# Kernel tuning notes

Hardware: AMD Instinct MI355X
Metric: run time of the kernel (lower is better)

The kernel has to match this reference:

```python
import jax, jax.numpy as jnp
import numpy as np

K = 7        # local attention window (kernel_size)
PAD = 3      # (K-1)//2, keeps spatial dims
GROUPS = 8   # attention heads


def _unfold(t, k, H, W):
    """t: [B,C,H+k-1,W+k-1] -> [B,C,H,W,k,k] sliding-window patches (stride 1).
    Matches torch .unfold(2,k,1).unfold(3,k,1): first k over height offsets,
    second k over width offsets."""
    cols = [t[:, :, i:i + H, j:j + W] for i in range(k) for j in range(k)]
    p = jnp.stack(cols, axis=-1)  # [B,C,H,W,k*k]
    return p.reshape(t.shape[0], t.shape[1], H, W, k, k)


def setup_inputs() -> dict:
    key = jax.random.key(0)
    ks = jax.random.split(key, 6)
    B, C, O, H, Wd = 4, 128, 128, 64, 64
    x = jax.random.normal(ks[0], (B, C, H, Wd), dtype=jnp.float32)
    # 1x1 conv weights, kaiming normal fan_out (fan_out = O for 1x1)
    scale = (2.0 / O) ** 0.5
    Wq = jax.random.normal(ks[1], (O, C), dtype=jnp.float32) * scale
    Wk = jax.random.normal(ks[2], (O, C), dtype=jnp.float32) * scale
    Wv = jax.random.normal(ks[3], (O, C), dtype=jnp.float32) * scale
    rel_h = jax.random.normal(ks[4], (O // 2, 1, 1, K, 1), dtype=jnp.float32)
    rel_w = jax.random.normal(ks[5], (O // 2, 1, 1, 1, K), dtype=jnp.float32)
    return {"x": x, "Wq": Wq, "Wk": Wk, "Wv": Wv, "rel_h": rel_h, "rel_w": rel_w}


def reference(x, Wq, Wk, Wv, rel_h, rel_w):
    B, C, H, W = x.shape
    O = Wq.shape[0]
    g = GROUPS
    # 1x1 convs (no bias)
    q = jnp.einsum('bchw,oc->bohw', x, Wq)                    # [B,O,H,W]
    xp = jnp.pad(x, ((0, 0), (0, 0), (PAD, PAD), (PAD, PAD)))
    k = jnp.einsum('bchw,oc->bohw', xp, Wk)                   # [B,O,Hp,Wp]
    v = jnp.einsum('bchw,oc->bohw', xp, Wv)
    kp = _unfold(k, K, H, W)                                  # [B,O,H,W,K,K]
    vp = _unfold(v, K, H, W)
    # relative position embeddings: height on first half of channels, width on second
    kh, kw = jnp.split(kp, 2, axis=1)
    kp = jnp.concatenate([kh + rel_h, kw + rel_w], axis=1)    # [B,O,H,W,K,K]
    kp = kp.reshape(B, g, O // g, H, W, K * K)
    vp = vp.reshape(B, g, O // g, H, W, K * K)
    qg = q.reshape(B, g, O // g, H, W, 1)
    scores = (qg * kp).sum(axis=2)                            # [B,g,H,W,K*K]
    attn = jax.nn.softmax(scores, axis=-1)
    out = jnp.einsum('bghwn,bgchwn->bgchw', attn, vp)         # [B,g,O/g,H,W]
    return out.reshape(B, O, H, W)
```

## Files before the change

kernel.cpp:

```cpp
#include <hip/hip_runtime.h>
#include <hip/hip_bf16.h>

#define B_   4
#define C_   128
#define H_   64
#define W_   64
#define HW_  4096
#define KW_  7
#define PAD_ 3
#define G_   8
#define CPG_ 16

#define CPAD 136

#define TS    16
#define HALO  22
#define NHP   (HALO*HALO)
#define LP    24

typedef _Float16 f16x8 __attribute__((ext_vector_type(8)));
typedef _Float16 h2    __attribute__((ext_vector_type(2)));
typedef float    f32x4 __attribute__((ext_vector_type(4)));

static __device__ __forceinline__ unsigned short f2h(float f) {
    _Float16 h = (_Float16)f;
    union { _Float16 h; unsigned short u; } cv; cv.h = h;
    return cv.u;
}

#if defined(__has_builtin)
#if __has_builtin(__builtin_amdgcn_fdot2)
#define HAVE_FDOT2 1
#endif
#endif

__global__ __launch_bounds__(256) void proj_mfma(
    const float* __restrict__ x,
    const float* __restrict__ Wq,
    const float* __restrict__ Wk,
    const float* __restrict__ Wv,
    unsigned short* __restrict__ qkv16)
{
    const int ptile = blockIdx.x;
    const int b     = blockIdx.y;
    const int m     = blockIdx.z;
    const float* Wm = (m == 0) ? Wq : ((m == 1) ? Wk : Wv);
    const float* xb = x + (size_t)b * C_ * HW_;
    unsigned short* y = qkv16 + ((size_t)(m * B_ + b)) * HW_ * C_;
    const int p0  = ptile * 64;
    const int tid = threadIdx.x;

    __shared__ unsigned short wls[128 * CPAD];
    __shared__ unsigned short xls[64 * CPAD];

    #pragma unroll
    for (int it = 0; it < 16; ++it) {
        const int idx = tid + it * 256;
        const int o   = idx >> 5;
        const int c4  = (idx & 31) * 4;
        const float4 w4 = *(const float4*)(Wm + (size_t)o * C_ + c4);
        ushort4 hh;
        hh.x = f2h(w4.x); hh.y = f2h(w4.y); hh.z = f2h(w4.z); hh.w = f2h(w4.w);
        *(ushort4*)(&wls[o * CPAD + c4]) = hh;
    }
    #pragma unroll
    for (int it = 0; it < 2; ++it) {
        const int idx = tid + it * 256;
        const int pq  = (idx & 15) * 4;
        const int cq  = (idx >> 4) * 4;
        const float* xp = xb + (size_t)cq * HW_ + p0 + pq;
        const float4 r0 = *(const float4*)(xp);
        const float4 r1 = *(const float4*)(xp + HW_);
        const float4 r2 = *(const float4*)(xp + 2 * HW_);
        const float4 r3 = *(const float4*)(xp + 3 * HW_);
        ushort4 hh;
        hh.x = f2h(r0.x); hh.y = f2h(r1.x); hh.z = f2h(r2.x); hh.w = f2h(r3.x);
        *(ushort4*)(&xls[(pq + 0) * CPAD + cq]) = hh;
        hh.x = f2h(r0.y); hh.y = f2h(r1.y); hh.z = f2h(r2.y); hh.w = f2h(r3.y);
        *(ushort4*)(&xls[(pq + 1) * CPAD + cq]) = hh;
        hh.x = f2h(r0.z); hh.y = f2h(r1.z); hh.z = f2h(r2.z); hh.w = f2h(r3.z);
        *(ushort4*)(&xls[(pq + 2) * CPAD + cq]) = hh;
        hh.x = f2h(r0.w); hh.y = f2h(r1.w); hh.z = f2h(r2.w); hh.w = f2h(r3.w);
        *(ushort4*)(&xls[(pq + 3) * CPAD + cq]) = hh;
    }
    __syncthreads();

    const int wv   = tid >> 6;
    const int lane = tid & 63;
    const int row  = lane & 15;
    const int kq   = lane >> 4;

    f32x4 acc[8];
    #pragma unroll
    for (int ot = 0; ot < 8; ++ot)
        acc[ot] = (f32x4){0.f, 0.f, 0.f, 0.f};

    #pragma unroll
    for (int ks = 0; ks < 4; ++ks) {
        const int cb = ks * 32 + kq * 8;
        const f16x8 bfrag = *(const f16x8*)(&xls[(wv * 16 + row) * CPAD + cb]);
        #pragma unroll
        for (int ot = 0; ot < 8; ++ot) {
            const f16x8 afrag = *(const f16x8*)(&wls[(ot * 16 + row) * CPAD + cb]);
            acc[ot] = __builtin_amdgcn_mfma_f32_16x16x32_f16(afrag, bfrag, acc[ot], 0, 0, 0);
        }
    }

    const int p = p0 + wv * 16 + row;
    #pragma unroll
    for (int ot = 0; ot < 8; ++ot) {
        ushort4 hh;
        hh.x = f2h(acc[ot][0]); hh.y = f2h(acc[ot][1]);
        hh.z = f2h(acc[ot][2]); hh.w = f2h(acc[ot][3]);
        *(ushort4*)(y + ((size_t)ot * HW_ + p) * CPG_ + kq * 4) = hh;
    }
}

__global__ __launch_bounds__(256) void attn_kernel(
    const unsigned short* __restrict__ qkv16,
    const float* __restrict__ rel_h,
    const float* __restrict__ rel_w,
    float* __restrict__ out)
{
    const int tile = blockIdx.x;
    const int g    = blockIdx.y;
    const int b    = blockIdx.z;
    const int h0   = (tile >> 2) * TS;
    const int w0   = (tile & 3) * TS;
    const int c0   = g * CPG_;

    __shared__ unsigned short kvls[2][NHP * LP];

    const size_t gplane = (size_t)HW_ * CPG_;
    const size_t mplane = (size_t)B_ * G_ * gplane;
    const unsigned short* qb = qkv16              + ((size_t)b * G_ + g) * gplane;
    const unsigned short* kb = qkv16 + mplane     + ((size_t)b * G_ + g) * gplane;
    const unsigned short* vb = qkv16 + 2 * mplane + ((size_t)b * G_ + g) * gplane;

    const int tid = threadIdx.x;
    const int pw  = tid & 15;
    const int ph  = tid >> 4;
    const int pix = (h0 + ph) * W_ + (w0 + pw);

    const f16x8 q0 = *(const f16x8*)(qb + (size_t)pix * CPG_);
    const f16x8 q1 = *(const f16x8*)(qb + (size_t)pix * CPG_ + 8);

    #pragma unroll
    for (int it = 0; it < 8; ++it) {
        const int idx = tid + it * 256;
        if (idx < 2 * NHP * 2) {
            const int arr  = (idx >= NHP * 2) ? 1 : 0;
            const int r    = idx - arr * NHP * 2;
            const int lp   = r >> 1;
            const int half = r & 1;
            const int hy   = h0 + lp / HALO - PAD_;
            const int hx   = w0 + lp % HALO - PAD_;
            f16x8 val = (f16x8)(_Float16)0.f;
            if ((unsigned)hy < (unsigned)H_ && (unsigned)hx < (unsigned)W_) {
                const unsigned short* src = (arr ? vb : kb)
                    + (size_t)(hy * W_ + hx) * CPG_ + half * 8;
                val = *(const f16x8*)src;
            }
            *(f16x8*)(&kvls[arr][lp * LP + half * 8]) = val;
        }
    }

    float qv[CPG_];
    #pragma unroll
    for (int c = 0; c < 8; ++c) { qv[c] = (float)q0[c]; qv[8 + c] = (float)q1[c]; }

    const bool useH = (g < 4);
    const float* rp = useH ? (rel_h + c0 * KW_) : (rel_w + (c0 - 64) * KW_);
    float rel[KW_];
    #pragma unroll
    for (int t = 0; t < KW_; ++t) {
        float r = 0.f;
        #pragma unroll
        for (int c = 0; c < CPG_; ++c) r += qv[c] * rp[c * KW_ + t];
        rel[t] = r;
    }

    __syncthreads();

    float s[KW_ * KW_];
    float smax = -1e30f;
    #pragma unroll
    for (int i = 0; i < KW_; ++i) {
        #pragma unroll
        for (int j = 0; j < KW_; ++j) {
            const unsigned short* kp = &kvls[0][((ph + i) * HALO + (pw + j)) * LP];
            const f16x8 k0 = *(const f16x8*)(kp);
            const f16x8 k1 = *(const f16x8*)(kp + 8);
            float sc = useH ? rel[i] : rel[j];
#ifdef HAVE_FDOT2
            #pragma unroll
            for (int t = 0; t < 4; ++t) {
                sc = __builtin_amdgcn_fdot2((h2){q0[2*t], q0[2*t+1]},
                                            (h2){k0[2*t], k0[2*t+1]}, sc, false);
                sc = __builtin_amdgcn_fdot2((h2){q1[2*t], q1[2*t+1]},
                                            (h2){k1[2*t], k1[2*t+1]}, sc, false);
            }
#else
            #pragma unroll
            for (int c = 0; c < 8; ++c)
                sc += qv[c] * (float)k0[c] + qv[8 + c] * (float)k1[c];
#endif
            s[i * KW_ + j] = sc;
            smax = fmaxf(smax, sc);
        }
    }

    float denom = 0.f;
    #pragma unroll
    for (int n = 0; n < KW_ * KW_; ++n) {
        s[n] = __expf(s[n] - smax);
        denom += s[n];
    }
    const float rdenom = 1.f / denom;

    float acc[CPG_];
    #pragma unroll
    for (int c = 0; c < CPG_; ++c) acc[c] = 0.f;
    #pragma unroll
    for (int i = 0; i < KW_; ++i) {
        #pragma unroll
        for (int j = 0; j < KW_; ++j) {
            const float a = s[i * KW_ + j];
            const unsigned short* vp = &kvls[1][((ph + i) * HALO + (pw + j)) * LP];
            const f16x8 v0 = *(const f16x8*)(vp);
            const f16x8 v1 = *(const f16x8*)(vp + 8);
            #pragma unroll
            for (int c = 0; c < 8; ++c) {
                acc[c]     += a * (float)v0[c];
                acc[8 + c] += a * (float)v1[c];
            }
        }
    }

    float* ob = out + ((size_t)b * C_ + c0) * HW_;
    #pragma unroll
    for (int c = 0; c < CPG_; ++c)
        ob[(size_t)c * HW_ + pix] = acc[c] * rdenom;
}

extern "C" void kernel_launch(void* const* d_in, const int* in_sizes, int n_in,
                              void* d_out, int out_size, void* d_ws, size_t ws_size,
                              hipStream_t stream) {
    const float* x     = (const float*)d_in[0];
    const float* Wq    = (const float*)d_in[1];
    const float* Wk    = (const float*)d_in[2];
    const float* Wv    = (const float*)d_in[3];
    const float* rel_h = (const float*)d_in[4];
    const float* rel_w = (const float*)d_in[5];
    unsigned short* ws = (unsigned short*)d_ws;
    float* out = (float*)d_out;

    dim3 gA(HW_ / 64, B_, 3);
    proj_mfma<<<gA, 256, 0, stream>>>(x, Wq, Wk, Wv, ws);

    dim3 gB(16, G_, B_);
    attn_kernel<<<gB, 256, 0, stream>>>(ws, rel_h, rel_w, out);
}
```

Baseline: 33.16 us.

## Compute two vertically adjacent pixels per thread to reuse K/V LDS loads

The attention kernel now uses 128 threads per block, with each thread handling two vertically adjacent output pixels. The K and V rows it loads from shared memory are reused across both pixels' overlapping 7x7 windows, cutting LDS reads per output roughly in half. In exchange, register use per thread roughly doubles (two score arrays and two accumulators) and there are fewer waves per block, which may lower occupancy or cause spills.

```diff
diff --git a/kernel.cpp b/kernel.cpp
--- a/kernel.cpp
+++ b/kernel.cpp
@@ -116,7 +116,7 @@
     }
 }
 
-__global__ __launch_bounds__(256) void attn_kernel(
+__global__ __launch_bounds__(128) void attn_kernel(
     const unsigned short* __restrict__ qkv16,
     const float* __restrict__ rel_h,
     const float* __restrict__ rel_w,
@@ -129,7 +129,8 @@
     const int w0   = (tile & 3) * TS;
     const int c0   = g * CPG_;
 
-    __shared__ unsigned short kvls[2][NHP * LP];
+    __shared__ unsigned short kls[NHP * LP];
+    __shared__ unsigned short vls[NHP * LP];
 
     const size_t gplane = (size_t)HW_ * CPG_;
     const size_t mplane = (size_t)B_ * G_ * gplane;
@@ -139,15 +140,19 @@
 
     const int tid = threadIdx.x;
     const int pw  = tid & 15;
-    const int ph  = tid >> 4;
-    const int pix = (h0 + ph) * W_ + (w0 + pw);
-
-    const f16x8 q0 = *(const f16x8*)(qb + (size_t)pix * CPG_);
-    const f16x8 q1 = *(const f16x8*)(qb + (size_t)pix * CPG_ + 8);
-
-    #pragma unroll
-    for (int it = 0; it < 8; ++it) {
-        const int idx = tid + it * 256;
+    const int php = tid >> 4;
+    const int row0 = 2 * php;
+    const int pix0 = (h0 + row0) * W_ + (w0 + pw);
+    const int pix1 = pix0 + W_;
+
+    const f16x8 q0a = *(const f16x8*)(qb + (size_t)pix0 * CPG_);
+    const f16x8 q0b = *(const f16x8*)(qb + (size_t)pix0 * CPG_ + 8);
+    const f16x8 q1a = *(const f16x8*)(qb + (size_t)pix1 * CPG_);
+    const f16x8 q1b = *(const f16x8*)(qb + (size_t)pix1 * CPG_ + 8);
+
+    #pragma unroll
+    for (int it = 0; it < 16; ++it) {
+        const int idx = tid + it * 128;
         if (idx < 2 * NHP * 2) {
             const int arr  = (idx >= NHP * 2) ? 1 : 0;
             const int r    = idx - arr * NHP * 2;
@@ -161,86 +166,184 @@
                     + (size_t)(hy * W_ + hx) * CPG_ + half * 8;
                 val = *(const f16x8*)src;
             }
-            *(f16x8*)(&kvls[arr][lp * LP + half * 8]) = val;
-        }
-    }
-
-    float qv[CPG_];
-    #pragma unroll
-    for (int c = 0; c < 8; ++c) { qv[c] = (float)q0[c]; qv[8 + c] = (float)q1[c]; }
+            unsigned short* dst = (arr ? vls : kls) + lp * LP + half * 8;
+            *(f16x8*)dst = val;
+        }
+    }
 
     const bool useH = (g < 4);
     const float* rp = useH ? (rel_h + c0 * KW_) : (rel_w + (c0 - 64) * KW_);
-    float rel[KW_];
-    #pragma unroll
-    for (int t = 0; t < KW_; ++t) {
-        float r = 0.f;
-        #pragma unroll
-        for (int c = 0; c < CPG_; ++c) r += qv[c] * rp[c * KW_ + t];
-        rel[t] = r;
+    float rel0[KW_], rel1[KW_];
+    {
+        float qv0[CPG_], qv1[CPG_];
+        #pragma unroll
+        for (int c = 0; c < 8; ++c) {
+            qv0[c] = (float)q0a[c]; qv0[8 + c] = (float)q0b[c];
+            qv1[c] = (float)q1a[c]; qv1[8 + c] = (float)q1b[c];
+        }
+        #pragma unroll
+        for (int t = 0; t < KW_; ++t) {
+            float r0 = 0.f, r1 = 0.f;
+            #pragma unroll
+            for (int c = 0; c < CPG_; ++c) {
+                const float w = rp[c * KW_ + t];
+                r0 += qv0[c] * w;
+                r1 += qv1[c] * w;
+            }
+            rel0[t] = r0; rel1[t] = r1;
+        }
     }
 
     __syncthreads();
 
-    float s[KW_ * KW_];
-    float smax = -1e30f;
-    #pragma unroll
-    for (int i = 0; i < KW_; ++i) {
+    float s0[KW_ * KW_], s1[KW_ * KW_];
+    #pragma unroll
+    for (int i = 0; i < KW_; ++i)
         #pragma unroll
         for (int j = 0; j < KW_; ++j) {
-            const unsigned short* kp = &kvls[0][((ph + i) * HALO + (pw + j)) * LP];
-            const f16x8 k0 = *(const f16x8*)(kp);
-            const f16x8 k1 = *(const f16x8*)(kp + 8);
-            float sc = useH ? rel[i] : rel[j];
+            s0[i * KW_ + j] = useH ? rel0[i] : rel0[j];
+            s1[i * KW_ + j] = useH ? rel1[i] : rel1[j];
+        }
+
+    #pragma unroll
+    for (int r = 0; r < 8; ++r) {
+        const int base = ((row0 + r) * HALO + pw) * LP;
+        {
+            f16x8 ka[KW_];
+            #pragma unroll
+            for (int t = 0; t < KW_; ++t)
+                ka[t] = *(const f16x8*)(&kls[base + t * LP]);
+            if (r < 7) {
+                #pragma unroll
+                for (int j = 0; j < KW_; ++j) {
+                    float sc = s0[r * KW_ + j];
 #ifdef HAVE_FDOT2
-            #pragma unroll
-            for (int t = 0; t < 4; ++t) {
-                sc = __builtin_amdgcn_fdot2((h2){q0[2*t], q0[2*t+1]},
-                                            (h2){k0[2*t], k0[2*t+1]}, sc, false);
-                sc = __builtin_amdgcn_fdot2((h2){q1[2*t], q1[2*t+1]},
-                                            (h2){k1[2*t], k1[2*t+1]}, sc, false);
-            }
+                    #pragma unroll
+                    for (int t = 0; t < 4; ++t)
+                        sc = __builtin_amdgcn_fdot2((h2){q0a[2*t], q0a[2*t+1]},
+                                                    (h2){ka[j][2*t], ka[j][2*t+1]}, sc, false);
 #else
-            #pragma unroll
-            for (int c = 0; c < 8; ++c)
-                sc += qv[c] * (float)k0[c] + qv[8 + c] * (float)k1[c];
-#endif
-            s[i * KW_ + j] = sc;
-            smax = fmaxf(smax, sc);
-        }
-    }
-
-    float denom = 0.f;
+                    #pragma unroll
+                    for (int c = 0; c < 8; ++c) sc += (float)q0a[c] * (float)ka[j][c];
+#endif
+                    s0[r * KW_ + j] = sc;
+                }
+            }
+            if (r >= 1) {
+                #pragma unroll
+                for (int j = 0; j < KW_; ++j) {
+                    float sc = s1[(r - 1) * KW_ + j];
+#ifdef HAVE_FDOT2
+                    #pragma unroll
+                    for (int t = 0; t < 4; ++t)
+                        sc = __builtin_amdgcn_fdot2((h2){q1a[2*t], q1a[2*t+1]},
+                                                    (h2){ka[j][2*t], ka[j][2*t+1]}, sc, false);
+#else
+                    #pragma unroll
+                    for (int c = 0; c < 8; ++c) sc += (float)q1a[c] * (float)ka[j][c];
+#endif
+                    s1[(r - 1) * KW_ + j] = sc;
+                }
+            }
+        }
+        {
+            f16x8 kb2[KW_];
+            #pragma unroll
+            for (int t = 0; t < KW_; ++t)
+                kb2[t] = *(const f16x8*)(&kls[base + t * LP + 8]);
+            if (r < 7) {
+                #pragma unroll
+                for (int j = 0; j < KW_; ++j) {
+                    float sc = s0[r * KW_ + j];
+#ifdef HAVE_FDOT2
+                    #pragma unroll
+                    for (int t = 0; t < 4; ++t)
+                        sc = __builtin_amdgcn_fdot2((h2){q0b[2*t], q0b[2*t+1]},
+                                                    (h2){kb2[j][2*t], kb2[j][2*t+1]}, sc, false);
+#else
+                    #pragma unroll
+                    for (int c = 0; c < 8; ++c) sc += (float)q0b[c] * (float)kb2[j][c];
+#endif
+                    s0[r * KW_ + j] = sc;
+                }
+            }
+            if (r >= 1) {
+                #pragma unroll
+                for (int j = 0; j < KW_; ++j) {
+                    float sc = s1[(r - 1) * KW_ + j];
+#ifdef HAVE_FDOT2
+                    #pragma unroll
+                    for (int t = 0; t < 4; ++t)
+                        sc = __builtin_amdgcn_fdot2((h2){q1b[2*t], q1b[2*t+1]},
+                                                    (h2){kb2[j][2*t], kb2[j][2*t+1]}, sc, false);
+#else
+                    #pragma unroll
+                    for (int c = 0; c < 8; ++c) sc += (float)q1b[c] * (float)kb2[j][c];
+#endif
+                    s1[(r - 1) * KW_ + j] = sc;
+                }
+            }
+        }
+    }
+
+    float smax0 = -1e30f, smax1 = -1e30f;
     #pragma unroll
     for (int n = 0; n < KW_ * KW_; ++n) {
-        s[n] = __expf(s[n] - smax);
-        denom += s[n];
-    }
-    const float rdenom = 1.f / denom;
-
-    float acc[CPG_];
-    #pragma unroll
-    for (int c = 0; c < CPG_; ++c) acc[c] = 0.f;
-    #pragma unroll
-    for (int i = 0; i < KW_; ++i) {
-        #pragma unroll
-        for (int j = 0; j < KW_; ++j) {
-            const float a = s[i * KW_ + j];
-            const unsigned short* vp = &kvls[1][((ph + i) * HALO + (pw + j)) * LP];
-            const f16x8 v0 = *(const f16x8*)(vp);
-            const f16x8 v1 = *(const f16x8*)(vp + 8);
-            #pragma unroll
-            for (int c = 0; c < 8; ++c) {
-                acc[c]     += a * (float)v0[c];
-                acc[8 + c] += a * (float)v1[c];
+        smax0 = fmaxf(smax0, s0[n]);
+        smax1 = fmaxf(smax1, s1[n]);
+    }
+    float den0 = 0.f, den1 = 0.f;
+    #pragma unroll
+    for (int n = 0; n < KW_ * KW_; ++n) {
+        s0[n] = __expf(s0[n] - smax0); den0 += s0[n];
+        s1[n] = __expf(s1[n] - smax1); den1 += s1[n];
+    }
+    const float rd0 = 1.f / den0;
+    const float rd1 = 1.f / den1;
+
+    float acc0[CPG_], acc1[CPG_];
+    #pragma unroll
+    for (int c = 0; c < CPG_; ++c) { acc0[c] = 0.f; acc1[c] = 0.f; }
+
+    #pragma unroll
+    for (int r = 0; r < 8; ++r) {
+        const int base = ((row0 + r) * HALO + pw) * LP;
+        f16x8 va[KW_], vb2[KW_];
+        #pragma unroll
+        for (int t = 0; t < KW_; ++t) {
+            va[t]  = *(const f16x8*)(&vls[base + t * LP]);
+            vb2[t] = *(const f16x8*)(&vls[base + t * LP + 8]);
+        }
+        if (r < 7) {
+            #pragma unroll
+            for (int j = 0; j < KW_; ++j) {
+                const float a = s0[r * KW_ + j];
+                #pragma unroll
+                for (int c = 0; c < 8; ++c) {
+                    acc0[c]     += a * (float)va[j][c];
+                    acc0[8 + c] += a * (float)vb2[j][c];
+                }
+            }
+        }
+        if (r >= 1) {
+            #pragma unroll
+            for (int j = 0; j < KW_; ++j) {
+                const float a = s1[(r - 1) * KW_ + j];
+                #pragma unroll
+                for (int c = 0; c < 8; ++c) {
+                    acc1[c]     += a * (float)va[j][c];
+                    acc1[8 + c] += a * (float)vb2[j][c];
+                }
             }
         }
     }
 
     float* ob = out + ((size_t)b * C_ + c0) * HW_;
     #pragma unroll
-    for (int c = 0; c < CPG_; ++c)
-        ob[(size_t)c * HW_ + pix] = acc[c] * rdenom;
+    for (int c = 0; c < CPG_; ++c) {
+        ob[(size_t)c * HW_ + pix0] = acc0[c] * rd0;
+        ob[(size_t)c * HW_ + pix1] = acc1[c] * rd1;
+    }
 }
 
 extern "C" void kernel_launch(void* const* d_in, const int* in_sizes, int n_in,
@@ -259,5 +362,5 @@
     proj_mfma<<<gA, 256, 0, stream>>>(x, Wq, Wk, Wv, ws);
 
     dim3 gB(16, G_, B_);
-    attn_kernel<<<gB, 256, 0, stream>>>(ws, rel_h, rel_w, out);
+    attn_kernel<<<gB, 128, 0, stream>>>(ws, rel_h, rel_w, out);
 }
```

Result: slower. 46.09 us (+39.0%).

## Use MFMA for local attention scores and value aggregation with padded V image

Applied to the files above, without the earlier changes.

Replaces the per-thread scalar QK dot products and softmax-weighted V accumulation with 16x16x16 f16 MFMA operations. Each window row is processed as a banded matrix with masks and an online softmax. V is now written by the projection kernel into a zero-padded channel-major image so tiles load without bounds checks, and the projection kernel also zeroes the border. The rel-position term is computed with a small MFMA. This adds masking overhead and wasted MFMA lanes outside the band, scattered 2-byte stores for V, and f16 rounding of the probabilities.

```diff
diff --git a/kernel.cpp b/kernel.cpp
--- a/kernel.cpp
+++ b/kernel.cpp
@@ -13,13 +13,15 @@
 
 #define CPAD 136
 
-#define TS    16
-#define HALO  22
-#define NHP   (HALO*HALO)
-#define LP    24
-
+#define TS     16
+#define HALOY  22
+#define KWP    24
+#define VWP    40
+#define IPITCH 80
+#define IROWS  72
+
+typedef _Float16 f16x4 __attribute__((ext_vector_type(4)));
 typedef _Float16 f16x8 __attribute__((ext_vector_type(8)));
-typedef _Float16 h2    __attribute__((ext_vector_type(2)));
 typedef float    f32x4 __attribute__((ext_vector_type(4)));
 
 static __device__ __forceinline__ unsigned short f2h(float f) {
@@ -27,19 +29,17 @@
     union { _Float16 h; unsigned short u; } cv; cv.h = h;
     return cv.u;
 }
-
-#if defined(__has_builtin)
-#if __has_builtin(__builtin_amdgcn_fdot2)
-#define HAVE_FDOT2 1
-#endif
-#endif
+static __device__ __forceinline__ float andf(float x, unsigned m) {
+    return __uint_as_float(__float_as_uint(x) & m);
+}
 
 __global__ __launch_bounds__(256) void proj_mfma(
     const float* __restrict__ x,
     const float* __restrict__ Wq,
     const float* __restrict__ Wk,
     const float* __restrict__ Wv,
-    unsigned short* __restrict__ qkv16)
+    unsigned short* __restrict__ qkv16,
+    unsigned short* __restrict__ v_img)
 {
     const int ptile = blockIdx.x;
     const int b     = blockIdx.y;
@@ -52,6 +52,23 @@
 
     __shared__ unsigned short wls[128 * CPAD];
     __shared__ unsigned short xls[64 * CPAD];
+
+    {
+        const int sid = (m * B_ + b) * 64 + ptile;
+        const long tot = 4L * 128 * 944;
+        long e = (long)sid * 630 + tid;
+        const long eend = min((long)(sid + 1) * 630, tot);
+        for (; e < eend; e += 256) {
+            const int bb  = (int)(e / (128L * 944));
+            const int rem = (int)(e - (long)bb * (128L * 944));
+            const int c   = rem / 944;
+            const int e2  = rem - c * 944;
+            int yy, xx;
+            if (e2 < 432) { const int k = e2 / 72; yy = (k < 3) ? k : 64 + k; xx = e2 - k * 72; }
+            else { const int e3 = e2 - 432; yy = 3 + (e3 >> 3); const int k = e3 & 7; xx = (k < 3) ? k : 64 + k; }
+            v_img[(((size_t)bb * 128 + c) * IROWS + yy) * IPITCH + xx] = 0;
+        }
+    }
 
     #pragma unroll
     for (int it = 0; it < 16; ++it) {
@@ -92,8 +109,7 @@
 
     f32x4 acc[8];
     #pragma unroll
-    for (int ot = 0; ot < 8; ++ot)
-        acc[ot] = (f32x4){0.f, 0.f, 0.f, 0.f};
+    for (int ot = 0; ot < 8; ++ot) acc[ot] = (f32x4){0.f, 0.f, 0.f, 0.f};
 
     #pragma unroll
     for (int ks = 0; ks < 4; ++ks) {
@@ -107,17 +123,29 @@
     }
 
     const int p = p0 + wv * 16 + row;
-    #pragma unroll
-    for (int ot = 0; ot < 8; ++ot) {
-        ushort4 hh;
-        hh.x = f2h(acc[ot][0]); hh.y = f2h(acc[ot][1]);
-        hh.z = f2h(acc[ot][2]); hh.w = f2h(acc[ot][3]);
-        *(ushort4*)(y + ((size_t)ot * HW_ + p) * CPG_ + kq * 4) = hh;
-    }
-}
-
-__global__ __launch_bounds__(256) void attn_kernel(
+    if (m < 2) {
+        #pragma unroll
+        for (int ot = 0; ot < 8; ++ot) {
+            ushort4 hh;
+            hh.x = f2h(acc[ot][0]); hh.y = f2h(acc[ot][1]);
+            hh.z = f2h(acc[ot][2]); hh.w = f2h(acc[ot][3]);
+            *(ushort4*)(y + ((size_t)ot * HW_ + p) * CPG_ + kq * 4) = hh;
+        }
+    } else {
+        const int iy = (p >> 6) + 3, ix = (p & 63) + 3;
+        #pragma unroll
+        for (int ot = 0; ot < 8; ++ot)
+            #pragma unroll
+            for (int r = 0; r < 4; ++r) {
+                const int o = ot * 16 + kq * 4 + r;
+                v_img[(((size_t)b * 128 + o) * IROWS + iy) * IPITCH + ix] = f2h(acc[ot][r]);
+            }
+    }
+}
+
+__global__ __launch_bounds__(256) void attn_mfma(
     const unsigned short* __restrict__ qkv16,
+    const unsigned short* __restrict__ v_img,
     const float* __restrict__ rel_h,
     const float* __restrict__ rel_w,
     float* __restrict__ out)
@@ -129,118 +157,144 @@
     const int w0   = (tile & 3) * TS;
     const int c0   = g * CPG_;
 
-    __shared__ unsigned short kvls[2][NHP * LP];
+    __shared__ unsigned short kls[HALOY * 32 * KWP];
+    __shared__ unsigned short vls[HALOY * 16 * VWP];
+    __shared__ unsigned short rpls[16 * 16];
 
     const size_t gplane = (size_t)HW_ * CPG_;
     const size_t mplane = (size_t)B_ * G_ * gplane;
-    const unsigned short* qb = qkv16              + ((size_t)b * G_ + g) * gplane;
-    const unsigned short* kb = qkv16 + mplane     + ((size_t)b * G_ + g) * gplane;
-    const unsigned short* vb = qkv16 + 2 * mplane + ((size_t)b * G_ + g) * gplane;
-
-    const int tid = threadIdx.x;
-    const int pw  = tid & 15;
-    const int ph  = tid >> 4;
-    const int pix = (h0 + ph) * W_ + (w0 + pw);
-
-    const f16x8 q0 = *(const f16x8*)(qb + (size_t)pix * CPG_);
-    const f16x8 q1 = *(const f16x8*)(qb + (size_t)pix * CPG_ + 8);
-
-    #pragma unroll
-    for (int it = 0; it < 8; ++it) {
-        const int idx = tid + it * 256;
-        if (idx < 2 * NHP * 2) {
-            const int arr  = (idx >= NHP * 2) ? 1 : 0;
-            const int r    = idx - arr * NHP * 2;
-            const int lp   = r >> 1;
-            const int half = r & 1;
-            const int hy   = h0 + lp / HALO - PAD_;
-            const int hx   = w0 + lp % HALO - PAD_;
-            f16x8 val = (f16x8)(_Float16)0.f;
-            if ((unsigned)hy < (unsigned)H_ && (unsigned)hx < (unsigned)W_) {
-                const unsigned short* src = (arr ? vb : kb)
-                    + (size_t)(hy * W_ + hx) * CPG_ + half * 8;
-                val = *(const f16x8*)src;
-            }
-            *(f16x8*)(&kvls[arr][lp * LP + half * 8]) = val;
-        }
-    }
-
-    float qv[CPG_];
-    #pragma unroll
-    for (int c = 0; c < 8; ++c) { qv[c] = (float)q0[c]; qv[8 + c] = (float)q1[c]; }
-
+    const unsigned short* qb = qkv16          + ((size_t)b * G_ + g) * gplane;
+    const unsigned short* kb = qkv16 + mplane + ((size_t)b * G_ + g) * gplane;
+    const unsigned short* vi = v_img + ((size_t)b * C_ + c0) * (IROWS * IPITCH);
+
+    const int tid  = threadIdx.x;
     const bool useH = (g < 4);
     const float* rp = useH ? (rel_h + c0 * KW_) : (rel_w + (c0 - 64) * KW_);
-    float rel[KW_];
-    #pragma unroll
-    for (int t = 0; t < KW_; ++t) {
-        float r = 0.f;
-        #pragma unroll
-        for (int c = 0; c < CPG_; ++c) r += qv[c] * rp[c * KW_ + t];
-        rel[t] = r;
-    }
-
+
+    {
+        const int j = tid >> 4, c = tid & 15;
+        rpls[j * 16 + c] = (j < KW_) ? f2h(rp[c * KW_ + j]) : (unsigned short)0;
+    }
+    #pragma unroll
+    for (int it = 0; it < 4; ++it) {
+        const int idx = tid + it * 256;
+        if (idx < 484 * 2) {
+            const int lp = idx >> 1, hf = idx & 1;
+            const int yy = lp / HALOY, ww = lp % HALOY;
+            const int ty = h0 + yy - PAD_, tx = w0 + ww - PAD_;
+            f16x8 val = (f16x8)(_Float16)0.f;
+            if ((unsigned)ty < (unsigned)H_ && (unsigned)tx < (unsigned)W_)
+                val = *(const f16x8*)(kb + (size_t)(ty * W_ + tx) * CPG_ + hf * 8);
+            *(f16x8*)(&kls[(yy * 32 + ww) * KWP + hf * 8]) = val;
+        }
+    }
+    #pragma unroll
+    for (int it = 0; it < 6; ++it) {
+        const int idx = tid + it * 256;
+        if (idx < 352 * 4) {
+            const int pq = idx >> 2, q4 = idx & 3;
+            const int yy = pq >> 4, cc = pq & 15;
+            f16x8 val = (f16x8)(_Float16)0.f;
+            if (q4 < 3)
+                val = *(const f16x8*)(vi + ((size_t)cc * IROWS + (h0 + yy)) * IPITCH + w0 + 8 * q4);
+            *(f16x8*)(&vls[(yy * 16 + cc) * VWP + 8 * q4]) = val;
+        }
+    }
     __syncthreads();
 
-    float s[KW_ * KW_];
-    float smax = -1e30f;
-    #pragma unroll
-    for (int i = 0; i < KW_; ++i) {
-        #pragma unroll
-        for (int j = 0; j < KW_; ++j) {
-            const unsigned short* kp = &kvls[0][((ph + i) * HALO + (pw + j)) * LP];
-            const f16x8 k0 = *(const f16x8*)(kp);
-            const f16x8 k1 = *(const f16x8*)(kp + 8);
-            float sc = useH ? rel[i] : rel[j];
-#ifdef HAVE_FDOT2
-            #pragma unroll
-            for (int t = 0; t < 4; ++t) {
-                sc = __builtin_amdgcn_fdot2((h2){q0[2*t], q0[2*t+1]},
-                                            (h2){k0[2*t], k0[2*t+1]}, sc, false);
-                sc = __builtin_amdgcn_fdot2((h2){q1[2*t], q1[2*t+1]},
-                                            (h2){k1[2*t], k1[2*t+1]}, sc, false);
+    const int lane = tid & 63, wv = tid >> 6;
+    const int l15 = lane & 15, wq = lane >> 4;
+
+    unsigned msk[8]; float nmk[8];
+    #pragma unroll
+    for (int r = 0; r < 4; ++r) {
+        const int jlo = 4 * wq + r - l15;
+        const int jhi = jlo + 16;
+        msk[r]     = ((unsigned)jlo <= 6u) ? 0xFFFFFFFFu : 0u;
+        msk[4 + r] = ((unsigned)jhi <= 6u) ? 0xFFFFFFFFu : 0u;
+        nmk[r]     = msk[r]     ? 0.f : -1e30f;
+        nmk[4 + r] = msk[4 + r] ? 0.f : -1e30f;
+    }
+
+    const f16x4 rfrag = *(const f16x4*)(&rpls[l15 * 16 + 4 * wq]);
+    float* obase = out + ((size_t)b * C_ + c0) * HW_;
+
+    for (int t = 0; t < 4; ++t) {
+        const int ph  = wv * 4 + t;
+        const int pix = (h0 + ph) * W_ + (w0 + l15);
+        const f16x4 qf = *(const f16x4*)(qb + (size_t)pix * CPG_ + 4 * wq);
+
+        const f32x4 rd = __builtin_amdgcn_mfma_f32_16x16x16f16(
+            rfrag, qf, (f32x4){0.f, 0.f, 0.f, 0.f}, 0, 0, 0);
+        float rl[KW_];
+        #pragma unroll
+        for (int j = 0; j < KW_; ++j)
+            rl[j] = __shfl(rd[j & 3], l15 + 16 * (j >> 2), 64);
+
+        float addW[8];
+        if (!useH) {
+            #pragma unroll
+            for (int r = 0; r < 8; ++r) {
+                const int j = 4 * wq + (r & 3) - l15 + ((r & 4) ? 16 : 0);
+                float v = -1e30f;
+                #pragma unroll
+                for (int jj = 0; jj < KW_; ++jj) v = (j == jj) ? rl[jj] : v;
+                addW[r] = v;
             }
-#else
-            #pragma unroll
-            for (int c = 0; c < 8; ++c)
-                sc += qv[c] * (float)k0[c] + qv[8 + c] * (float)k1[c];
-#endif
-            s[i * KW_ + j] = sc;
-            smax = fmaxf(smax, sc);
-        }
-    }
-
-    float denom = 0.f;
-    #pragma unroll
-    for (int n = 0; n < KW_ * KW_; ++n) {
-        s[n] = __expf(s[n] - smax);
-        denom += s[n];
-    }
-    const float rdenom = 1.f / denom;
-
-    float acc[CPG_];
-    #pragma unroll
-    for (int c = 0; c < CPG_; ++c) acc[c] = 0.f;
-    #pragma unroll
-    for (int i = 0; i < KW_; ++i) {
-        #pragma unroll
-        for (int j = 0; j < KW_; ++j) {
-            const float a = s[i * KW_ + j];
-            const unsigned short* vp = &kvls[1][((ph + i) * HALO + (pw + j)) * LP];
-            const f16x8 v0 = *(const f16x8*)(vp);
-            const f16x8 v1 = *(const f16x8*)(vp + 8);
-            #pragma unroll
-            for (int c = 0; c < 8; ++c) {
-                acc[c]     += a * (float)v0[c];
-                acc[8 + c] += a * (float)v1[c];
+        }
+
+        f32x4 Cacc = {0.f, 0.f, 0.f, 0.f};
+        float m = -1e30f, lsum = 0.f;
+
+        #pragma unroll
+        for (int i = 0; i < KW_; ++i) {
+            const int yy = ph + i;
+            const int kbase = yy * 32 * KWP;
+            const f16x4 klo = *(const f16x4*)(&kls[kbase + l15 * KWP + 4 * wq]);
+            const f16x4 khi = *(const f16x4*)(&kls[kbase + (16 + l15) * KWP + 4 * wq]);
+            const f32x4 S1 = __builtin_amdgcn_mfma_f32_16x16x16f16(
+                klo, qf, (f32x4){0.f, 0.f, 0.f, 0.f}, 0, 0, 0);
+            const f32x4 S2 = __builtin_amdgcn_mfma_f32_16x16x16f16(
+                khi, qf, (f32x4){0.f, 0.f, 0.f, 0.f}, 0, 0, 0);
+
+            float sp[8];
+            #pragma unroll
+            for (int r = 0; r < 8; ++r) {
+                const float s = (r < 4) ? S1[r] : S2[r - 4];
+                sp[r] = useH ? (andf(s + rl[i], msk[r]) + nmk[r])
+                             : (andf(s, msk[r]) + addW[r]);
             }
-        }
-    }
-
-    float* ob = out + ((size_t)b * C_ + c0) * HW_;
-    #pragma unroll
-    for (int c = 0; c < CPG_; ++c)
-        ob[(size_t)c * HW_ + pix] = acc[c] * rdenom;
+            float tm = sp[0];
+            #pragma unroll
+            for (int r = 1; r < 8; ++r) tm = fmaxf(tm, sp[r]);
+            tm = fmaxf(tm, __shfl_xor(tm, 16, 64));
+            tm = fmaxf(tm, __shfl_xor(tm, 32, 64));
+            const float mnew  = fmaxf(m, tm);
+            const float alpha = __expf(m - mnew);
+            m = mnew; lsum *= alpha;
+            #pragma unroll
+            for (int r = 0; r < 4; ++r) Cacc[r] *= alpha;
+
+            float pv[8];
+            #pragma unroll
+            for (int r = 0; r < 8; ++r) { pv[r] = __expf(sp[r] - mnew); lsum += pv[r]; }
+            const f16x4 plo = {(_Float16)pv[0], (_Float16)pv[1], (_Float16)pv[2], (_Float16)pv[3]};
+            const f16x4 phi = {(_Float16)pv[4], (_Float16)pv[5], (_Float16)pv[6], (_Float16)pv[7]};
+
+            const int vbase = (yy * 16 + l15) * VWP;
+            const f16x4 vlo = *(const f16x4*)(&vls[vbase + 4 * wq]);
+            const f16x4 vhi = *(const f16x4*)(&vls[vbase + 16 + 4 * wq]);
+            Cacc = __builtin_amdgcn_mfma_f32_16x16x16f16(vlo, plo, Cacc, 0, 0, 0);
+            Cacc = __builtin_amdgcn_mfma_f32_16x16x16f16(vhi, phi, Cacc, 0, 0, 0);
+        }
+
+        float l2 = lsum + __shfl_xor(lsum, 16, 64);
+        l2 = l2 + __shfl_xor(l2, 32, 64);
+        const float rden = 1.f / l2;
+        #pragma unroll
+        for (int r = 0; r < 4; ++r)
+            obase[(size_t)(4 * wq + r) * HW_ + pix] = Cacc[r] * rden;
+    }
 }
 
 extern "C" void kernel_launch(void* const* d_in, const int* in_sizes, int n_in,
@@ -252,12 +306,14 @@
     const float* Wv    = (const float*)d_in[3];
     const float* rel_h = (const float*)d_in[4];
     const float* rel_w = (const float*)d_in[5];
-    unsigned short* ws = (unsigned short*)d_ws;
+    unsigned short* ws    = (unsigned short*)d_ws;
+    unsigned short* qkv   = ws;
+    unsigned short* v_img = ws + (size_t)3 * B_ * HW_ * C_;
     float* out = (float*)d_out;
 
     dim3 gA(HW_ / 64, B_, 3);
-    proj_mfma<<<gA, 256, 0, stream>>>(x, Wq, Wk, Wv, ws);
+    proj_mfma<<<gA, 256, 0, stream>>>(x, Wq, Wk, Wv, qkv, v_img);
 
     dim3 gB(16, G_, B_);
-    attn_kernel<<<gB, 256, 0, stream>>>(ws, rel_h, rel_w, out);
-}
+    attn_mfma<<<gB, 256, 0, stream>>>(qkv, v_img, rel_h, rel_w, out);
+}
```

After: 40.78 us. 23.0% more time.
